# Kernel optimization log

Hardware: AMD Instinct MI355X
Metric: run time of the kernel (lower is better)

## Reference

```python
import jax, jax.numpy as jnp
import numpy as np

N_EMBD = 1024
HEAD_SIZE = 64
BLOCK_SIZE = 512
BATCH = 4


def setup_inputs() -> dict:
    key = jax.random.key(0)
    ks = jax.random.split(key, 5)
    T = BLOCK_SIZE
    x = jax.random.normal(ks[0], (BATCH, 2 * T - 1, N_EMBD), dtype=jnp.float32)
    scale = 1.0 / np.sqrt(N_EMBD)
    Wk = jax.random.normal(ks[1], (N_EMBD, HEAD_SIZE), dtype=jnp.float32) * scale
    Wv = jax.random.normal(ks[2], (N_EMBD, HEAD_SIZE), dtype=jnp.float32) * scale
    Wq = jax.random.normal(ks[3], (N_EMBD, HEAD_SIZE), dtype=jnp.float32) * scale
    # keyWindowBias in torch has shape (1,1,head_size,block_size); store as (hs, T)
    bias = jax.random.normal(ks[4], (HEAD_SIZE, T), dtype=jnp.float32)
    return {"x": x, "Wk": Wk, "Wv": Wv, "Wq": Wq, "bias": bias}


def reference(x, Wk, Wv, Wq, bias):
    B, S, C = x.shape
    T = (S + 1) // 2  # S == 2*T - 1 (block_size)
    xToPred = x[:, -T:, :]
    # block_layer == 0 path: project full sequence for k, v
    k = jnp.einsum('bsc,cd->bsd', x, Wk)        # [B, 2T-1, hs]
    v = jnp.einsum('bsc,cd->bsd', x, Wv)        # [B, 2T-1, hs]
    q = jnp.einsum('btc,cd->btd', xToPred, Wq)  # [B, T, hs]

    # sliding windows: window w covers positions w..w+T-1 (torch unfold semantics)
    idx = jnp.arange(T)[:, None] + jnp.arange(T)[None, :]  # [T, T]

    k_win = k[:, idx, :] + bias.T[None, None, :, :]  # [B, T, T, hs] + [1,1,T,hs]
    wei = jnp.einsum('bwd,bwtd->bwt', q, k_win)      # [B, T, T]
    wei = jax.nn.softmax(wei, axis=-1)

    v_win = v[:, idx, :]                              # [B, T, T, hs]
    out = jnp.einsum('bwt,bwtd->bwd', wei, v_win)     # [B, T, hs]
    return out
```

## Files before the change

### kernel.cpp

```cpp
#include <hip/hip_runtime.h>
#include <hip/hip_bf16.h>

#define BB 4
#define SS 1023
#define TT 512
#define CC 1024
#define DD 64
#define NROW (BB*SS)
#define NROWP 4096

typedef float f4 __attribute__((ext_vector_type(4)));
typedef float f2 __attribute__((ext_vector_type(2)));
typedef short bf16x8 __attribute__((ext_vector_type(8)));
typedef float f32x4 __attribute__((ext_vector_type(4)));

__device__ __forceinline__ unsigned split_rtn(float v) {
    const unsigned u  = __builtin_bit_cast(unsigned, v);
    const unsigned r  = u + 0x7FFFu + ((u >> 16) & 1u);
    const unsigned hi = r >> 16;
    const float hif   = __builtin_bit_cast(float, r & 0xFFFF0000u);
    const float res   = v - hif;
    const unsigned u2 = __builtin_bit_cast(unsigned, res);
    const unsigned r2 = u2 + 0x7FFFu + ((u2 >> 16) & 1u);
    return (r2 & 0xFFFF0000u) | hi;
}

__global__ __launch_bounds__(64) void wsplit_kernel(
    const float* __restrict__ Wk,
    const float* __restrict__ Wv,
    const float* __restrict__ Wq,
    unsigned short* __restrict__ bwh,
    unsigned short* __restrict__ bwl)
{
    const int f    = blockIdx.x;
    const int p    = f >> 7;
    const int rem  = f & 127;
    const int nsub = rem >> 5;
    const int ks   = rem & 31;
    const int lane = threadIdx.x;
    const int quad = lane >> 4, l4 = lane & 15;
    const float* W = (p == 0) ? Wk : (p == 1) ? Wv : Wq;
    const int n = nsub * 16 + l4;

    bf16x8 h, l;
#pragma unroll
    for (int j = 0; j < 8; ++j) {
        const int k = ks * 32 + quad * 8 + j;
        const unsigned hl = split_rtn(W[k * DD + n]);
        h[j] = (short)(hl & 0xFFFFu);
        l[j] = (short)(hl >> 16);
    }
    ((bf16x8*)bwh)[f * 64 + lane] = h;
    ((bf16x8*)bwl)[f * 64 + lane] = l;
}

__global__ __launch_bounds__(64) void proj_mfma_kernel(
    const float* __restrict__ x,
    const unsigned short* __restrict__ bwh,
    const unsigned short* __restrict__ bwl,
    float* __restrict__ kT,
    float* __restrict__ vbuf,
    float* __restrict__ qbuf)
{
    const int blk  = blockIdx.x;
    const int nh   = blk & 1;
    const int pm   = blk >> 1;
    const int p    = pm % 3;
    const int mt   = pm / 3;
    const int bs0  = mt * 16;
    const int lane = threadIdx.x;
    const int quad = lane >> 4, l4 = lane & 15;
    const int nsub0 = nh * 2;

    int arow = bs0 + l4; if (arow > NROW - 1) arow = NROW - 1;
    const float* ap = x + (size_t)arow * CC;
    const bf16x8* bh = (const bf16x8*)bwh
                     + (size_t)((p * 4 + nsub0) * 32) * 64 + lane;
    const bf16x8* bl = (const bf16x8*)bwl
                     + (size_t)((p * 4 + nsub0) * 32) * 64 + lane;

    f32x4 acc0 = {0.f,0.f,0.f,0.f}, acc1 = {0.f,0.f,0.f,0.f};

#pragma unroll 4
    for (int ks = 0; ks < 32; ++ks) {
        const int k0 = ks * 32 + quad * 8;
        const f4 xa = *(const f4*)(ap + k0);
        const f4 xb = *(const f4*)(ap + k0 + 4);
        bf16x8 ah, al;
#pragma unroll
        for (int j = 0; j < 4; ++j) {
            const unsigned hl = split_rtn(xa[j]);
            ah[j] = (short)(hl & 0xFFFFu);
            al[j] = (short)(hl >> 16);
        }
#pragma unroll
        for (int j = 0; j < 4; ++j) {
            const unsigned hl = split_rtn(xb[j]);
            ah[4 + j] = (short)(hl & 0xFFFFu);
            al[4 + j] = (short)(hl >> 16);
        }
        const bf16x8 bh0 = bh[(0 * 32 + ks) * 64];
        const bf16x8 bh1 = bh[(1 * 32 + ks) * 64];
        const bf16x8 bl0 = bl[(0 * 32 + ks) * 64];
        const bf16x8 bl1 = bl[(1 * 32 + ks) * 64];

        acc0 = __builtin_amdgcn_mfma_f32_16x16x32_bf16(ah, bh0, acc0, 0, 0, 0);
        acc1 = __builtin_amdgcn_mfma_f32_16x16x32_bf16(ah, bh1, acc1, 0, 0, 0);
        acc0 = __builtin_amdgcn_mfma_f32_16x16x32_bf16(ah, bl0, acc0, 0, 0, 0);
        acc1 = __builtin_amdgcn_mfma_f32_16x16x32_bf16(ah, bl1, acc1, 0, 0, 0);
        acc0 = __builtin_amdgcn_mfma_f32_16x16x32_bf16(al, bh0, acc0, 0, 0, 0);
        acc1 = __builtin_amdgcn_mfma_f32_16x16x32_bf16(al, bh1, acc1, 0, 0, 0);
        acc0 = __builtin_amdgcn_mfma_f32_16x16x32_bf16(al, bl0, acc0, 0, 0, 0);
        acc1 = __builtin_amdgcn_mfma_f32_16x16x32_bf16(al, bl1, acc1, 0, 0, 0);
    }

#pragma unroll
    for (int s = 0; s < 2; ++s) {
        const f32x4 a = s ? acc1 : acc0;
        const int d = (nsub0 + s) * 16 + l4;
#pragma unroll
        for (int reg = 0; reg < 4; ++reg) {
            const int bs = bs0 + quad * 4 + reg;
            if (bs < NROW) {
                const float val = a[reg];
                const int b = bs / SS, ss = bs - b * SS;
                if (p == 0) {
                    kT[(size_t)d * NROWP + b * 1024 + ss] = val;
                } else if (p == 1) {
                    vbuf[(size_t)bs * DD + d] = val;
                } else {
                    if (ss >= TT - 1)
                        qbuf[((size_t)b * TT + (ss - (TT - 1))) * DD + d] = val;
                }
            }
        }
    }
}

__global__ __launch_bounds__(512) void qbias_kernel(
    const float* __restrict__ qbuf,
    const float* __restrict__ bias,
    float* __restrict__ qb)
{
    __shared__ __align__(16) float qsT[DD][4];

    const int tid = threadIdx.x;
    const int blk = blockIdx.x;
    const int b   = blk >> 7;
    const int w0  = (blk & 127) * 4;

    if (tid < 4 * DD) {
        const int m = tid >> 6, dd = tid & 63;
        qsT[dd][m] = qbuf[((size_t)b * TT + w0 + m) * DD + dd];
    }
    __syncthreads();

    const int t = tid;
    f4 acc = {0.f, 0.f, 0.f, 0.f};
#pragma unroll 8
    for (int dd = 0; dd < DD; ++dd) {
        const float bb = bias[dd * TT + t];
        const f4 qv = *(const f4*)&qsT[dd][0];
        acc[0] = fmaf(qv[0], bb, acc[0]);
        acc[1] = fmaf(qv[1], bb, acc[1]);
        acc[2] = fmaf(qv[2], bb, acc[2]);
        acc[3] = fmaf(qv[3], bb, acc[3]);
    }
#pragma unroll
    for (int m = 0; m < 4; ++m)
        qb[((size_t)b * TT + w0 + m) * TT + t] = acc[m];
}

__global__ __launch_bounds__(512) void attn_kernel(
    const float* __restrict__ kT,
    const float* __restrict__ vbuf,
    const float* __restrict__ qbuf,
    const float* __restrict__ qb,
    float* __restrict__ out)
{
    __shared__ __align__(8) float qsT[DD][2];
    __shared__ __align__(8) float part[2][2][TT];
    __shared__ __align__(8) float weiT[TT][2];
    __shared__ float red[16];
    __shared__ float invs[2];
    __shared__ float partial[8][2][DD];

    const int tid  = threadIdx.x;
    const int lane = tid & 63;
    const int wv   = tid >> 6;
    const int blk  = blockIdx.x;
    const int b    = blk >> 8;
    const int w0   = (blk & 255) * 2;

    if (tid < 2 * DD) {
        const int m = tid >> 6, dd = tid & 63;
        qsT[dd][m] = qbuf[((size_t)b * TT + w0 + m) * DD + dd];
    }
    __syncthreads();

    {
        const int h = tid >> 8, p = tid & 255;
        const int t0 = 2 * p;
        const float* kcol = kT + (size_t)(32 * h) * NROWP + b * 1024 + w0 + t0;
        float a00, a01, a10, a11;
        if (h == 0) {
            const float* qbp = qb + ((size_t)b * TT + w0) * TT + t0;
            const f2 q0v = *(const f2*)qbp;
            const f2 q1v = *(const f2*)(qbp + TT);
            a00 = q0v[0]; a01 = q0v[1]; a10 = q1v[0]; a11 = q1v[1];
        } else {
            a00 = a01 = a10 = a11 = 0.f;
        }
#pragma unroll 8
        for (int i = 0; i < 32; ++i) {
            const int dd = 32 * h + i;
            const float* kr = kcol + (size_t)i * NROWP;
            const f2 kA = *(const f2*)kr;
            const f2 kB = *(const f2*)(kr + 2);
            const float q0 = qsT[dd][0], q1 = qsT[dd][1];
            a00 = fmaf(q0, kA[0], a00);
            a01 = fmaf(q0, kA[1], a01);
            a10 = fmaf(q1, kA[1], a10);
            a11 = fmaf(q1, kB[0], a11);
        }
        *(f2*)&part[h][0][t0] = (f2){a00, a01};
        *(f2*)&part[h][1][t0] = (f2){a10, a11};
    }
    __syncthreads();

    {
        const int m = wv >> 2, qt = wv & 3;
        const int tb = qt * 128 + lane;
        float r0 = part[0][m][tb]      + part[1][m][tb];
        float r1 = part[0][m][tb + 64] + part[1][m][tb + 64];
        float mx = fmaxf(r0, r1);
#pragma unroll
        for (int off = 1; off < 64; off <<= 1)
            mx = fmaxf(mx, __shfl_xor(mx, off, 64));
        if (lane == 0) red[wv] = mx;
        __syncthreads();
        mx = fmaxf(fmaxf(red[m * 4], red[m * 4 + 1]),
                   fmaxf(red[m * 4 + 2], red[m * 4 + 3]));
        const float e0 = __expf(r0 - mx), e1 = __expf(r1 - mx);
        weiT[tb][m] = e0;
        weiT[tb + 64][m] = e1;
        float sum = e0 + e1;
#pragma unroll
        for (int off = 1; off < 64; off <<= 1)
            sum += __shfl_xor(sum, off, 64);
        if (lane == 0) red[8 + wv] = sum;
        __syncthreads();
        if (tid < 2)
            invs[tid] = 1.f / (red[8 + tid * 4] + red[9 + tid * 4] +
                               red[10 + tid * 4] + red[11 + tid * 4]);
    }
    __syncthreads();

    {
        const int t0r = wv * 64;
        const float* vb = vbuf + ((size_t)b * SS + w0 + t0r) * DD + lane;
        float p0 = 0.f, p1 = 0.f;
        float v0 = vb[0];
#pragma unroll 4
        for (int t = 0; t < 64; ++t) {
            const float v1 = vb[(size_t)(t + 1) * DD];
            const f2 w2 = *(const f2*)&weiT[t0r + t][0];
            p0 = fmaf(w2[0], v0, p0);
            p1 = fmaf(w2[1], v1, p1);
            v0 = v1;
        }
        partial[wv][0][lane] = p0;
        partial[wv][1][lane] = p1;
    }
    __syncthreads();

    if (tid < 2 * DD) {
        const int m = tid >> 6, dd = tid & 63;
        float o = 0.f;
#pragma unroll
        for (int j = 0; j < 8; ++j) o += partial[j][m][dd];
        out[((size_t)b * TT + w0 + m) * DD + dd] = o * invs[m];
    }
}

extern "C" void kernel_launch(void* const* d_in, const int* in_sizes, int n_in,
                              void* d_out, int out_size, void* d_ws, size_t ws_size,
                              hipStream_t stream) {
    const float* x    = (const float*)d_in[0];
    const float* Wk   = (const float*)d_in[1];
    const float* Wv   = (const float*)d_in[2];
    const float* Wq   = (const float*)d_in[3];
    const float* bias = (const float*)d_in[4];
    float* out = (float*)d_out;

    char* ws = (char*)d_ws;
    float* kT             = (float*)(ws + 0);
    float* vbuf           = (float*)(ws + (2u  << 20));
    float* qbuf           = (float*)(ws + (4u  << 20));
    float* qb             = (float*)(ws + (8u  << 20));
    unsigned short* bwh   = (unsigned short*)(ws + (16u << 20));
    unsigned short* bwl   = (unsigned short*)(ws + (20u << 20));

    wsplit_kernel<<<384, 64, 0, stream>>>(Wk, Wv, Wq, bwh, bwl);
    proj_mfma_kernel<<<1536, 64, 0, stream>>>(x, bwh, bwl, kT, vbuf, qbuf);
    qbias_kernel<<<BB * TT / 4, 512, 0, stream>>>(qbuf, bias, qb);
    attn_kernel<<<BB * TT / 2, 512, 0, stream>>>(kT, vbuf, qbuf, qb, out);
}
```

Before: 119.2 us.

## Pre-split x into bf16 hi/lo once, widen projection tiles, fuse bias into attention

The fp32-to-bf16 hi/lo split of x now runs once in a combined split kernel and is written to workspace. Before, each projection block recomputed it, six times per row tile. The projection kernel now computes all four 16-column subtiles per block, halving the grid and reusing the A fragments. The separate q·bias kernel and its qb buffer are removed, and the bias term is accumulated inside the attention score loop. This costs extra global traffic for the split x buffers and extra bias loads and FMAs in the attention kernel.

```diff
diff --git a/kernel.cpp b/kernel.cpp
--- a/kernel.cpp
+++ b/kernel.cpp
@@ -25,37 +25,72 @@
     return (r2 & 0xFFFF0000u) | hi;
 }
 
-__global__ __launch_bounds__(64) void wsplit_kernel(
+__global__ __launch_bounds__(64) void split_kernel(
     const float* __restrict__ Wk,
     const float* __restrict__ Wv,
     const float* __restrict__ Wq,
+    const float* __restrict__ x,
     unsigned short* __restrict__ bwh,
-    unsigned short* __restrict__ bwl)
+    unsigned short* __restrict__ bwl,
+    unsigned short* __restrict__ xh,
+    unsigned short* __restrict__ xl)
 {
-    const int f    = blockIdx.x;
-    const int p    = f >> 7;
-    const int rem  = f & 127;
-    const int nsub = rem >> 5;
-    const int ks   = rem & 31;
     const int lane = threadIdx.x;
     const int quad = lane >> 4, l4 = lane & 15;
-    const float* W = (p == 0) ? Wk : (p == 1) ? Wv : Wq;
-    const int n = nsub * 16 + l4;
-
-    bf16x8 h, l;
-#pragma unroll
-    for (int j = 0; j < 8; ++j) {
-        const int k = ks * 32 + quad * 8 + j;
-        const unsigned hl = split_rtn(W[k * DD + n]);
-        h[j] = (short)(hl & 0xFFFFu);
-        l[j] = (short)(hl >> 16);
-    }
-    ((bf16x8*)bwh)[f * 64 + lane] = h;
-    ((bf16x8*)bwl)[f * 64 + lane] = l;
+
+    if (blockIdx.x < 384) {
+        const int f    = blockIdx.x;
+        const int p    = f >> 7;
+        const int rem  = f & 127;
+        const int nsub = rem >> 5;
+        const int ks   = rem & 31;
+        const float* W = (p == 0) ? Wk : (p == 1) ? Wv : Wq;
+        const int n = nsub * 16 + l4;
+
+        bf16x8 h, l;
+#pragma unroll
+        for (int j = 0; j < 8; ++j) {
+            const int k = ks * 32 + quad * 8 + j;
+            const unsigned hl = split_rtn(W[k * DD + n]);
+            h[j] = (short)(hl & 0xFFFFu);
+            l[j] = (short)(hl >> 16);
+        }
+        ((bf16x8*)bwh)[f * 64 + lane] = h;
+        ((bf16x8*)bwl)[f * 64 + lane] = l;
+    } else {
+        const int mt = blockIdx.x - 384;
+        int arow = mt * 16 + l4; if (arow > NROW - 1) arow = NROW - 1;
+        const float* ap = x + (size_t)arow * CC;
+        bf16x8* oh = (bf16x8*)xh + (size_t)(mt * 32) * 64 + lane;
+        bf16x8* ol = (bf16x8*)xl + (size_t)(mt * 32) * 64 + lane;
+
+#pragma unroll 4
+        for (int ks = 0; ks < 32; ++ks) {
+            const int k0 = ks * 32 + quad * 8;
+            const f4 xa = *(const f4*)(ap + k0);
+            const f4 xb = *(const f4*)(ap + k0 + 4);
+            bf16x8 h, l;
+#pragma unroll
+            for (int j = 0; j < 4; ++j) {
+                const unsigned hl = split_rtn(xa[j]);
+                h[j] = (short)(hl & 0xFFFFu);
+                l[j] = (short)(hl >> 16);
+            }
+#pragma unroll
+            for (int j = 0; j < 4; ++j) {
+                const unsigned hl = split_rtn(xb[j]);
+                h[4 + j] = (short)(hl & 0xFFFFu);
+                l[4 + j] = (short)(hl >> 16);
+            }
+            oh[ks * 64] = h;
+            ol[ks * 64] = l;
+        }
+    }
 }
 
 __global__ __launch_bounds__(64) void proj_mfma_kernel(
-    const float* __restrict__ x,
+    const unsigned short* __restrict__ xh,
+    const unsigned short* __restrict__ xl,
     const unsigned short* __restrict__ bwh,
     const unsigned short* __restrict__ bwl,
     float* __restrict__ kT,
@@ -63,61 +98,40 @@
     float* __restrict__ qbuf)
 {
     const int blk  = blockIdx.x;
-    const int nh   = blk & 1;
-    const int pm   = blk >> 1;
-    const int p    = pm % 3;
-    const int mt   = pm / 3;
+    const int p    = blk % 3;
+    const int mt   = blk / 3;
     const int bs0  = mt * 16;
     const int lane = threadIdx.x;
     const int quad = lane >> 4, l4 = lane & 15;
-    const int nsub0 = nh * 2;
-
-    int arow = bs0 + l4; if (arow > NROW - 1) arow = NROW - 1;
-    const float* ap = x + (size_t)arow * CC;
-    const bf16x8* bh = (const bf16x8*)bwh
-                     + (size_t)((p * 4 + nsub0) * 32) * 64 + lane;
-    const bf16x8* bl = (const bf16x8*)bwl
-                     + (size_t)((p * 4 + nsub0) * 32) * 64 + lane;
-
-    f32x4 acc0 = {0.f,0.f,0.f,0.f}, acc1 = {0.f,0.f,0.f,0.f};
-
-#pragma unroll 4
+
+    const bf16x8* xhp = (const bf16x8*)xh + (size_t)(mt * 32) * 64 + lane;
+    const bf16x8* xlp = (const bf16x8*)xl + (size_t)(mt * 32) * 64 + lane;
+    const bf16x8* bh  = (const bf16x8*)bwh + (size_t)(p * 4 * 32) * 64 + lane;
+    const bf16x8* bl  = (const bf16x8*)bwl + (size_t)(p * 4 * 32) * 64 + lane;
+
+    f32x4 acc[4];
+#pragma unroll
+    for (int n = 0; n < 4; ++n) acc[n] = (f32x4){0.f, 0.f, 0.f, 0.f};
+
+#pragma unroll 2
     for (int ks = 0; ks < 32; ++ks) {
-        const int k0 = ks * 32 + quad * 8;
-        const f4 xa = *(const f4*)(ap + k0);
-        const f4 xb = *(const f4*)(ap + k0 + 4);
-        bf16x8 ah, al;
-#pragma unroll
-        for (int j = 0; j < 4; ++j) {
-            const unsigned hl = split_rtn(xa[j]);
-            ah[j] = (short)(hl & 0xFFFFu);
-            al[j] = (short)(hl >> 16);
-        }
-#pragma unroll
-        for (int j = 0; j < 4; ++j) {
-            const unsigned hl = split_rtn(xb[j]);
-            ah[4 + j] = (short)(hl & 0xFFFFu);
-            al[4 + j] = (short)(hl >> 16);
-        }
-        const bf16x8 bh0 = bh[(0 * 32 + ks) * 64];
-        const bf16x8 bh1 = bh[(1 * 32 + ks) * 64];
-        const bf16x8 bl0 = bl[(0 * 32 + ks) * 64];
-        const bf16x8 bl1 = bl[(1 * 32 + ks) * 64];
-
-        acc0 = __builtin_amdgcn_mfma_f32_16x16x32_bf16(ah, bh0, acc0, 0, 0, 0);
-        acc1 = __builtin_amdgcn_mfma_f32_16x16x32_bf16(ah, bh1, acc1, 0, 0, 0);
-        acc0 = __builtin_amdgcn_mfma_f32_16x16x32_bf16(ah, bl0, acc0, 0, 0, 0);
-        acc1 = __builtin_amdgcn_mfma_f32_16x16x32_bf16(ah, bl1, acc1, 0, 0, 0);
-        acc0 = __builtin_amdgcn_mfma_f32_16x16x32_bf16(al, bh0, acc0, 0, 0, 0);
-        acc1 = __builtin_amdgcn_mfma_f32_16x16x32_bf16(al, bh1, acc1, 0, 0, 0);
-        acc0 = __builtin_amdgcn_mfma_f32_16x16x32_bf16(al, bl0, acc0, 0, 0, 0);
-        acc1 = __builtin_amdgcn_mfma_f32_16x16x32_bf16(al, bl1, acc1, 0, 0, 0);
-    }
-
-#pragma unroll
-    for (int s = 0; s < 2; ++s) {
-        const f32x4 a = s ? acc1 : acc0;
-        const int d = (nsub0 + s) * 16 + l4;
+        const bf16x8 ah = xhp[ks * 64];
+        const bf16x8 al = xlp[ks * 64];
+#pragma unroll
+        for (int n = 0; n < 4; ++n) {
+            const bf16x8 bhn = bh[(n * 32 + ks) * 64];
+            const bf16x8 bln = bl[(n * 32 + ks) * 64];
+            acc[n] = __builtin_amdgcn_mfma_f32_16x16x32_bf16(ah, bhn, acc[n], 0, 0, 0);
+            acc[n] = __builtin_amdgcn_mfma_f32_16x16x32_bf16(ah, bln, acc[n], 0, 0, 0);
+            acc[n] = __builtin_amdgcn_mfma_f32_16x16x32_bf16(al, bhn, acc[n], 0, 0, 0);
+            acc[n] = __builtin_amdgcn_mfma_f32_16x16x32_bf16(al, bln, acc[n], 0, 0, 0);
+        }
+    }
+
+#pragma unroll
+    for (int s = 0; s < 4; ++s) {
+        const f32x4 a = acc[s];
+        const int d = s * 16 + l4;
 #pragma unroll
         for (int reg = 0; reg < 4; ++reg) {
             const int bs = bs0 + quad * 4 + reg;
@@ -137,45 +151,11 @@
     }
 }
 
-__global__ __launch_bounds__(512) void qbias_kernel(
-    const float* __restrict__ qbuf,
-    const float* __restrict__ bias,
-    float* __restrict__ qb)
-{
-    __shared__ __align__(16) float qsT[DD][4];
-
-    const int tid = threadIdx.x;
-    const int blk = blockIdx.x;
-    const int b   = blk >> 7;
-    const int w0  = (blk & 127) * 4;
-
-    if (tid < 4 * DD) {
-        const int m = tid >> 6, dd = tid & 63;
-        qsT[dd][m] = qbuf[((size_t)b * TT + w0 + m) * DD + dd];
-    }
-    __syncthreads();
-
-    const int t = tid;
-    f4 acc = {0.f, 0.f, 0.f, 0.f};
-#pragma unroll 8
-    for (int dd = 0; dd < DD; ++dd) {
-        const float bb = bias[dd * TT + t];
-        const f4 qv = *(const f4*)&qsT[dd][0];
-        acc[0] = fmaf(qv[0], bb, acc[0]);
-        acc[1] = fmaf(qv[1], bb, acc[1]);
-        acc[2] = fmaf(qv[2], bb, acc[2]);
-        acc[3] = fmaf(qv[3], bb, acc[3]);
-    }
-#pragma unroll
-    for (int m = 0; m < 4; ++m)
-        qb[((size_t)b * TT + w0 + m) * TT + t] = acc[m];
-}
-
 __global__ __launch_bounds__(512) void attn_kernel(
     const float* __restrict__ kT,
     const float* __restrict__ vbuf,
     const float* __restrict__ qbuf,
-    const float* __restrict__ qb,
+    const float* __restrict__ bias,
     float* __restrict__ out)
 {
     __shared__ __align__(8) float qsT[DD][2];
@@ -202,26 +182,23 @@
         const int h = tid >> 8, p = tid & 255;
         const int t0 = 2 * p;
         const float* kcol = kT + (size_t)(32 * h) * NROWP + b * 1024 + w0 + t0;
-        float a00, a01, a10, a11;
-        if (h == 0) {
-            const float* qbp = qb + ((size_t)b * TT + w0) * TT + t0;
-            const f2 q0v = *(const f2*)qbp;
-            const f2 q1v = *(const f2*)(qbp + TT);
-            a00 = q0v[0]; a01 = q0v[1]; a10 = q1v[0]; a11 = q1v[1];
-        } else {
-            a00 = a01 = a10 = a11 = 0.f;
-        }
+        const float* bp   = bias + (size_t)(32 * h) * TT + t0;
+        float a00 = 0.f, a01 = 0.f, a10 = 0.f, a11 = 0.f;
 #pragma unroll 8
         for (int i = 0; i < 32; ++i) {
-            const int dd = 32 * h + i;
             const float* kr = kcol + (size_t)i * NROWP;
             const f2 kA = *(const f2*)kr;
-            const f2 kB = *(const f2*)(kr + 2);
-            const float q0 = qsT[dd][0], q1 = qsT[dd][1];
-            a00 = fmaf(q0, kA[0], a00);
-            a01 = fmaf(q0, kA[1], a01);
-            a10 = fmaf(q1, kA[1], a10);
-            a11 = fmaf(q1, kB[0], a11);
+            const float kC = kr[2];
+            const f2 bv = *(const f2*)(bp + (size_t)i * TT);
+            const f2 qv = *(const f2*)&qsT[32 * h + i][0];
+            a00 = fmaf(qv[0], kA[0], a00);
+            a01 = fmaf(qv[0], kA[1], a01);
+            a10 = fmaf(qv[1], kA[1], a10);
+            a11 = fmaf(qv[1], kC,    a11);
+            a00 = fmaf(qv[0], bv[0], a00);
+            a01 = fmaf(qv[0], bv[1], a01);
+            a10 = fmaf(qv[1], bv[0], a10);
+            a11 = fmaf(qv[1], bv[1], a11);
         }
         *(f2*)&part[h][0][t0] = (f2){a00, a01};
         *(f2*)&part[h][1][t0] = (f2){a10, a11};
@@ -297,12 +274,12 @@
     float* kT             = (float*)(ws + 0);
     float* vbuf           = (float*)(ws + (2u  << 20));
     float* qbuf           = (float*)(ws + (4u  << 20));
-    float* qb             = (float*)(ws + (8u  << 20));
-    unsigned short* bwh   = (unsigned short*)(ws + (16u << 20));
-    unsigned short* bwl   = (unsigned short*)(ws + (20u << 20));
-
-    wsplit_kernel<<<384, 64, 0, stream>>>(Wk, Wv, Wq, bwh, bwl);
-    proj_mfma_kernel<<<1536, 64, 0, stream>>>(x, bwh, bwl, kT, vbuf, qbuf);
-    qbias_kernel<<<BB * TT / 4, 512, 0, stream>>>(qbuf, bias, qb);
-    attn_kernel<<<BB * TT / 2, 512, 0, stream>>>(kT, vbuf, qbuf, qb, out);
-}
+    unsigned short* bwh   = (unsigned short*)(ws + (6u  << 20));
+    unsigned short* bwl   = (unsigned short*)(ws + (8u  << 20));
+    unsigned short* xh    = (unsigned short*)(ws + (10u << 20));
+    unsigned short* xl    = (unsigned short*)(ws + (20u << 20));
+
+    split_kernel<<<640, 64, 0, stream>>>(Wk, Wv, Wq, x, bwh, bwl, xh, xl);
+    proj_mfma_kernel<<<768, 64, 0, stream>>>(xh, xl, bwh, bwl, kT, vbuf, qbuf);
+    attn_kernel<<<BB * TT / 2, 512, 0, stream>>>(kT, vbuf, qbuf, bias, out);
+}
```

After: 123.5 us. +3.6%, slower.
